# Kernel optimization log

Measured on AMD Instinct MI355X. Metric: run time of the kernel, lower is better.

The kernel has to match this reference:

```python
import jax, jax.numpy as jnp
import numpy as np
import math

# Config constants (from init_kwargs)
KV_CHANNELS = 128
NUM_HEADS = 32
NUM_KV_HEADS = 2
LAYER_NUMBER = 2  # apply_query_key_layer_scaling=True -> coeff = layer_number
HEAD_DIM = KV_CHANNELS
HIDDEN = KV_CHANNELS * NUM_HEADS
COEFF = float(LAYER_NUMBER)
NORM_FACTOR = math.sqrt(HEAD_DIM) * COEFF


def setup_inputs() -> dict:
    key = jax.random.key(0)
    k1, k2, k3, k4 = jax.random.split(key, 4)
    B, Q, KV = 2, 2048, 2048
    query_layer = jax.random.normal(k1, (B, NUM_HEADS, Q, HEAD_DIM), dtype=jnp.float32)
    key_layer = jax.random.normal(k2, (B, NUM_KV_HEADS, KV, HEAD_DIM), dtype=jnp.float32)
    value_layer = jax.random.normal(k3, (B, NUM_KV_HEADS, KV, HEAD_DIM), dtype=jnp.float32)
    attention_mask = jax.random.normal(k4, (B, 1, Q, KV), dtype=jnp.float32)
    return {
        "query_layer": query_layer,
        "key_layer": key_layer,
        "value_layer": value_layer,
        "attention_mask": attention_mask,
    }


def reference(query_layer, key_layer, value_layer, attention_mask):
    # Fallback (non-FusedSDPA) path of CoreAttention.forward, eval mode (no dropout).
    b, h, q_len, d = query_layer.shape
    g = key_layer.shape[1]          # num_key_value_heads
    r = h // g                      # n_rep
    # gaudi_chatglm_repeat_kv: grouped view (b, g, r, q, d) vs kv (b, g, kv, d)
    qg = query_layer.reshape(b, g, r, q_len, d)
    # scores: (b, g, r, q, kv)
    scores = jnp.einsum("bgrqd,bgkd->bgrqk", qg, key_layer) / NORM_FACTOR
    scores = scores * COEFF
    # mask unsqueezed at dim 1 -> (b, 1, 1, q, kv), broadcast-add
    scores = scores + attention_mask[:, None]
    # softmax in fp32, cast back to query dtype
    attn = jax.nn.softmax(scores.astype(jnp.float32), axis=-1).astype(query_layer.dtype)
    # AV: (b, g, r, q, d)
    out = jnp.einsum("bgrqk,bgkd->bgrqd", attn, value_layer)
    out = out.reshape(b, h, q_len, d)
    # permute (2,0,1,3) -> (q, b, h, d); reshape -> (q, b, hidden)
    context = jnp.transpose(out, (2, 0, 1, 3)).reshape(q_len, b, h * d)
    return context
```

## Files before the change

kernel.cpp:

```cpp
#include <hip/hip_runtime.h>
#include <hip/hip_bf16.h>


constexpr int Bn = 2, Hn = 32, Gn = 2, Qn = 2048, KVn = 2048, Dn = 128;
constexpr int WAVES = 8, QBLK = 32, HO = 8;
constexpr int KVB = 32, NT = KVn / KVB;
constexpr int NT32 = KVn / 32;
constexpr float SCALE = 0.08838834764831843f;
constexpr float L2E = 1.4426950408889634f;
constexpr float SCALE2 = SCALE * L2E;

constexpr size_t WSK_BYTES = (size_t)Bn * Gn * KVn * 256;

typedef __attribute__((ext_vector_type(16))) float f32x16;
typedef __attribute__((ext_vector_type(8))) __bf16 bf16x8;

__device__ __forceinline__ unsigned pk2(float a, float b) {
  union { __bf16 h[2]; unsigned u; } x;
  x.h[0] = (__bf16)a; x.h[1] = (__bf16)b;
  return x.u;
}

__global__ __launch_bounds__(256)
void prepack(const float* __restrict__ Kg, const float* __restrict__ Vg,
             char* __restrict__ wsK, char* __restrict__ wsV) {
  const int i = blockIdx.x * 256 + threadIdx.x;
  {
    const int dp = i & 63, kv = (i >> 6) & (KVn - 1), bg = i >> 17;
    const float* src = Kg + ((size_t)bg * KVn + kv) * Dn + 2 * dp;
    const unsigned pr = pk2(src[0], src[1]);
    const size_t off = (size_t)bg * (KVn * 256) + (size_t)kv * 256
                       + ((4 * dp) ^ ((kv & 15) << 4));
    *(unsigned*)(wsK + off) = pr;
  }
  {
    const int d = i & 127, vg = (i >> 7) & 1023, bg = i >> 17;
    const int t = vg >> 4, vkp = vg & 15;
    const float* src = Vg + ((size_t)bg * KVn + t * 32 + 2 * vkp) * Dn + d;
    const unsigned pr = pk2(src[0], src[Dn]);
    const int slot = (((d >> 3) ^ (d >> 1)) & 3) << 4;
    const size_t off = ((size_t)bg * NT32 + t) * 8192 + (d << 6)
                       + ((vkp * 4) ^ slot);
    *(unsigned*)(wsV + off) = pr;
  }
}

__global__ __launch_bounds__(512, 2)
void attn_fwd(const float* __restrict__ Qg, const float* __restrict__ Mg,
              const char* __restrict__ wsK, const char* __restrict__ wsV,
              float* __restrict__ Og) {
  __shared__ __align__(16) short Ks[2][KVB * Dn];
  __shared__ __align__(16) short Vt[2][Dn * KVB];
  __shared__ __align__(16) float Ms[2][QBLK * KVB];

  const int tid = threadIdx.x;
  const int lane = tid & 63, w = tid >> 6;
  const int hi = lane >> 5, ln = lane & 31;
  const int qb = blockIdx.x * QBLK, ho = blockIdx.y, b = blockIdx.z;
  const int h = ho * HO + w;
  const int g = ho >> 1, bg = b * Gn + g;

  bf16x8 aq[8];
  {
    const float* qr = Qg + ((size_t)(b * Hn + h) * Qn + qb + ln) * Dn + hi * 8;
#pragma unroll
    for (int ks = 0; ks < 8; ++ks) {
      float4 f0 = *(const float4*)(qr + ks * 16);
      float4 f1 = *(const float4*)(qr + ks * 16 + 4);
      union { unsigned u[4]; bf16x8 b; } t;
      t.u[0] = pk2(f0.x * SCALE2, f0.y * SCALE2);
      t.u[1] = pk2(f0.z * SCALE2, f0.w * SCALE2);
      t.u[2] = pk2(f1.x * SCALE2, f1.y * SCALE2);
      t.u[3] = pk2(f1.z * SCALE2, f1.w * SCALE2);
      aq[ks] = t.b;
    }
  }

  const char* wsKb = wsK + (size_t)bg * (KVn * 256);
  const char* wsVb = wsV + (size_t)bg * (KVn * 256);
  const int mr = (w & 3) * 8 + (lane >> 3);
  const int mc = (lane & 7) << 4;
  const char* mSrcBase = (const char*)Mg + (size_t)(b * Qn + qb + mr) * (KVn * 4)
                         + (mc ^ ((mr & 7) << 4));

  auto stage = [&](int tile, int buf) {
    if (w < 4) {
      const char* sk = wsKb + (size_t)tile * 8192 + w * 2048 + lane * 16;
      char* dk = (char*)Ks[buf] + w * 2048;
      __builtin_amdgcn_global_load_lds(
          (const __attribute__((address_space(1))) void*)sk,
          (__attribute__((address_space(3))) void*)dk, 16, 0, 0);
      __builtin_amdgcn_global_load_lds(
          (const __attribute__((address_space(1))) void*)(sk + 1024),
          (__attribute__((address_space(3))) void*)(dk + 1024), 16, 0, 0);
      const char* sm = mSrcBase + tile * 128;
      char* dm = (char*)Ms[buf] + w * 1024;
      __builtin_amdgcn_global_load_lds(
          (const __attribute__((address_space(1))) void*)sm,
          (__attribute__((address_space(3))) void*)dm, 16, 0, 0);
    } else {
      const int wv = w - 4;
      const char* sv = wsVb + (size_t)tile * 8192 + wv * 2048 + lane * 16;
      char* dv = (char*)Vt[buf] + wv * 2048;
      __builtin_amdgcn_global_load_lds(
          (const __attribute__((address_space(1))) void*)sv,
          (__attribute__((address_space(3))) void*)dv, 16, 0, 0);
      __builtin_amdgcn_global_load_lds(
          (const __attribute__((address_space(1))) void*)(sv + 1024),
          (__attribute__((address_space(3))) void*)(dv + 1024), 16, 0, 0);
    }
  };

  f32x16 o[4];
#pragma unroll
  for (int nt = 0; nt < 4; ++nt)
#pragma unroll
    for (int e = 0; e < 16; ++e) o[nt][e] = 0.0f;
  float lsum = 0.0f;

  stage(0, 0);
  __syncthreads();

  const int ksw = (ln & 15) << 4;
  const int msw = (ln & 7) << 4;

  for (int t = 0; t < NT; ++t) {
    const int cur = t & 1;
    const int tn = (t + 1 < NT) ? t + 1 : t;

    stage(tn, cur ^ 1);
    __builtin_amdgcn_sched_barrier(0);

    f32x16 s;
#pragma unroll
    for (int e = 0; e < 16; ++e) s[e] = 0.0f;
    const char* ksb = (const char*)Ks[cur];
    __builtin_amdgcn_s_setprio(1);
#pragma unroll
    for (int ks = 0; ks < 8; ++ks) {
      bf16x8 k0 = *(const bf16x8*)(ksb + (ln << 8) + ((ks * 32 + hi * 16) ^ ksw));
      s = __builtin_amdgcn_mfma_f32_32x32x16_bf16(k0, aq[ks], s, 0, 0, 0);
    }
    __builtin_amdgcn_s_setprio(0);

    const char* msb = (const char*)Ms[cur] + ln * 128;
    unsigned own[8];
    float psum = 0.0f;
#pragma unroll
    for (int gq = 0; gq < 4; ++gq) {
      float4 mkq = *(const float4*)(msb + ((gq * 32 + hi * 16) ^ msw));
      float p0 = __builtin_exp2f(__builtin_fmaf(mkq.x, L2E, s[4 * gq + 0]));
      float p1 = __builtin_exp2f(__builtin_fmaf(mkq.y, L2E, s[4 * gq + 1]));
      float p2 = __builtin_exp2f(__builtin_fmaf(mkq.z, L2E, s[4 * gq + 2]));
      float p3 = __builtin_exp2f(__builtin_fmaf(mkq.w, L2E, s[4 * gq + 3]));
      psum += (p0 + p1) + (p2 + p3);
      own[2 * gq] = pk2(p0, p1);
      own[2 * gq + 1] = pk2(p2, p3);
    }
    lsum += psum;

    unsigned sw[8];
#pragma unroll
    for (int i = 0; i < 8; ++i) sw[i] = __shfl_xor(own[i], 32);
    union Frag { unsigned u[4]; bf16x8 b; };
    Frag pf[2];
#pragma unroll
    for (int ks = 0; ks < 2; ++ks) {
      const int bsl = ks * 4;
      pf[ks].u[0] = hi ? sw[bsl + 2] : own[bsl + 0];
      pf[ks].u[1] = hi ? sw[bsl + 3] : own[bsl + 1];
      pf[ks].u[2] = hi ? own[bsl + 2] : sw[bsl + 0];
      pf[ks].u[3] = hi ? own[bsl + 3] : sw[bsl + 1];
    }

    const char* vtb = (const char*)Vt[cur];
    __builtin_amdgcn_s_setprio(1);
#pragma unroll
    for (int nt = 0; nt < 4; ++nt) {
      const int d = nt * 32 + ln;
      const int swz = (((d >> 3) ^ (d >> 1)) & 3) << 4;
#pragma unroll
      for (int ks = 0; ks < 2; ++ks) {
        bf16x8 vfr = *(const bf16x8*)(vtb + (d << 6) + (((ks * 32 + hi * 16)) ^ swz));
        o[nt] = __builtin_amdgcn_mfma_f32_32x32x16_bf16(vfr, pf[ks].b, o[nt], 0, 0, 0);
      }
    }
    __builtin_amdgcn_s_setprio(0);

    __syncthreads();
  }

  const float ltot = lsum + __shfl_xor(lsum, 32);
  const float invl = 1.0f / ltot;
  float* outp = Og + (size_t)(qb + ln) * (Bn * Hn * Dn) + (size_t)b * (Hn * Dn) + h * Dn;
#pragma unroll
  for (int nt = 0; nt < 4; ++nt)
#pragma unroll
    for (int gq = 0; gq < 4; ++gq) {
      float4 v;
      v.x = o[nt][gq * 4 + 0] * invl;
      v.y = o[nt][gq * 4 + 1] * invl;
      v.z = o[nt][gq * 4 + 2] * invl;
      v.w = o[nt][gq * 4 + 3] * invl;
      *(float4*)(outp + nt * 32 + gq * 8 + hi * 4) = v;
    }
}

extern "C" void kernel_launch(void* const* d_in, const int* in_sizes, int n_in,
                              void* d_out, int out_size, void* d_ws, size_t ws_size,
                              hipStream_t stream) {
  const float* q = (const float*)d_in[0];
  const float* k = (const float*)d_in[1];
  const float* v = (const float*)d_in[2];
  const float* m = (const float*)d_in[3];
  float* out = (float*)d_out;
  char* wsK = (char*)d_ws;
  char* wsV = wsK + WSK_BYTES;

  prepack<<<dim3((Bn * Gn * KVn * 64) / 256), 256, 0, stream>>>(k, v, wsK, wsV);
  dim3 grid(Qn / QBLK, Hn / HO, Bn);
  attn_fwd<<<grid, WAVES * 64, 0, stream>>>(q, m, wsK, wsV, out);
}
```

Measured before the change: 229.8 us.

## Double KV tile to 64 per iteration and use permlane32_swap for P fragments

Raises the KV tile processed per loop iteration from 32 to 64, halving the number of iterations and block-wide barriers. Every wave now stages K, V and mask slices instead of splitting roles. The two QK score accumulators are computed back to back, exposing more independent MFMA work. The lane-half exchange for P fragments uses the permlane32_swap builtin when available in place of shfl_xor plus selects. Shared memory doubles to about 64 KB per block, which may limit occupancy at the two-blocks-per-CU launch bound, and register pressure rises.

```diff
diff --git a/kernel.cpp b/kernel.cpp
--- a/kernel.cpp
+++ b/kernel.cpp
@@ -4,7 +4,7 @@
 
 constexpr int Bn = 2, Hn = 32, Gn = 2, Qn = 2048, KVn = 2048, Dn = 128;
 constexpr int WAVES = 8, QBLK = 32, HO = 8;
-constexpr int KVB = 32, NT = KVn / KVB;
+constexpr int KVB = 64, NT = KVn / KVB;
 constexpr int NT32 = KVn / 32;
 constexpr float SCALE = 0.08838834764831843f;
 constexpr float L2E = 1.4426950408889634f;
@@ -14,6 +14,7 @@
 
 typedef __attribute__((ext_vector_type(16))) float f32x16;
 typedef __attribute__((ext_vector_type(8))) __bf16 bf16x8;
+typedef __attribute__((ext_vector_type(2))) unsigned u32x2;
 
 __device__ __forceinline__ unsigned pk2(float a, float b) {
   union { __bf16 h[2]; unsigned u; } x;
@@ -78,37 +79,33 @@
 
   const char* wsKb = wsK + (size_t)bg * (KVn * 256);
   const char* wsVb = wsV + (size_t)bg * (KVn * 256);
-  const int mr = (w & 3) * 8 + (lane >> 3);
-  const int mc = (lane & 7) << 4;
+  const int mr = w * 4 + (lane >> 4);
+  const int mc = (lane & 15) << 4;
   const char* mSrcBase = (const char*)Mg + (size_t)(b * Qn + qb + mr) * (KVn * 4)
-                         + (mc ^ ((mr & 7) << 4));
+                         + (mc ^ ((mr & 15) << 4));
 
   auto stage = [&](int tile, int buf) {
-    if (w < 4) {
-      const char* sk = wsKb + (size_t)tile * 8192 + w * 2048 + lane * 16;
-      char* dk = (char*)Ks[buf] + w * 2048;
-      __builtin_amdgcn_global_load_lds(
-          (const __attribute__((address_space(1))) void*)sk,
-          (__attribute__((address_space(3))) void*)dk, 16, 0, 0);
-      __builtin_amdgcn_global_load_lds(
-          (const __attribute__((address_space(1))) void*)(sk + 1024),
-          (__attribute__((address_space(3))) void*)(dk + 1024), 16, 0, 0);
-      const char* sm = mSrcBase + tile * 128;
-      char* dm = (char*)Ms[buf] + w * 1024;
-      __builtin_amdgcn_global_load_lds(
-          (const __attribute__((address_space(1))) void*)sm,
-          (__attribute__((address_space(3))) void*)dm, 16, 0, 0);
-    } else {
-      const int wv = w - 4;
-      const char* sv = wsVb + (size_t)tile * 8192 + wv * 2048 + lane * 16;
-      char* dv = (char*)Vt[buf] + wv * 2048;
-      __builtin_amdgcn_global_load_lds(
-          (const __attribute__((address_space(1))) void*)sv,
-          (__attribute__((address_space(3))) void*)dv, 16, 0, 0);
-      __builtin_amdgcn_global_load_lds(
-          (const __attribute__((address_space(1))) void*)(sv + 1024),
-          (__attribute__((address_space(3))) void*)(dv + 1024), 16, 0, 0);
-    }
+    const char* sk = wsKb + (size_t)tile * 16384 + w * 2048 + lane * 16;
+    char* dk = (char*)Ks[buf] + w * 2048;
+    __builtin_amdgcn_global_load_lds(
+        (const __attribute__((address_space(1))) void*)sk,
+        (__attribute__((address_space(3))) void*)dk, 16, 0, 0);
+    __builtin_amdgcn_global_load_lds(
+        (const __attribute__((address_space(1))) void*)(sk + 1024),
+        (__attribute__((address_space(3))) void*)(dk + 1024), 16, 0, 0);
+    const char* sv = wsVb + (size_t)tile * 16384 + w * 2048 + lane * 16;
+    char* dv = (char*)Vt[buf] + w * 2048;
+    __builtin_amdgcn_global_load_lds(
+        (const __attribute__((address_space(1))) void*)sv,
+        (__attribute__((address_space(3))) void*)dv, 16, 0, 0);
+    __builtin_amdgcn_global_load_lds(
+        (const __attribute__((address_space(1))) void*)(sv + 1024),
+        (__attribute__((address_space(3))) void*)(dv + 1024), 16, 0, 0);
+    const char* sm = mSrcBase + tile * 256;
+    char* dm = (char*)Ms[buf] + w * 1024;
+    __builtin_amdgcn_global_load_lds(
+        (const __attribute__((address_space(1))) void*)sm,
+        (__attribute__((address_space(3))) void*)dm, 16, 0, 0);
   };
 
   f32x16 o[4];
@@ -122,7 +119,7 @@
   __syncthreads();
 
   const int ksw = (ln & 15) << 4;
-  const int msw = (ln & 7) << 4;
+  const int msw = (ln & 15) << 4;
 
   for (int t = 0; t < NT; ++t) {
     const int cur = t & 1;
@@ -131,46 +128,61 @@
     stage(tn, cur ^ 1);
     __builtin_amdgcn_sched_barrier(0);
 
-    f32x16 s;
-#pragma unroll
-    for (int e = 0; e < 16; ++e) s[e] = 0.0f;
+    f32x16 s0, s1;
+#pragma unroll
+    for (int e = 0; e < 16; ++e) { s0[e] = 0.0f; s1[e] = 0.0f; }
     const char* ksb = (const char*)Ks[cur];
     __builtin_amdgcn_s_setprio(1);
 #pragma unroll
     for (int ks = 0; ks < 8; ++ks) {
-      bf16x8 k0 = *(const bf16x8*)(ksb + (ln << 8) + ((ks * 32 + hi * 16) ^ ksw));
-      s = __builtin_amdgcn_mfma_f32_32x32x16_bf16(k0, aq[ks], s, 0, 0, 0);
+      const int byte = (ks * 32 + hi * 16) ^ ksw;
+      bf16x8 k0 = *(const bf16x8*)(ksb + (ln << 8) + byte);
+      bf16x8 k1 = *(const bf16x8*)(ksb + ((32 + ln) << 8) + byte);
+      s0 = __builtin_amdgcn_mfma_f32_32x32x16_bf16(k0, aq[ks], s0, 0, 0, 0);
+      s1 = __builtin_amdgcn_mfma_f32_32x32x16_bf16(k1, aq[ks], s1, 0, 0, 0);
     }
     __builtin_amdgcn_s_setprio(0);
 
-    const char* msb = (const char*)Ms[cur] + ln * 128;
-    unsigned own[8];
+    const char* msb = (const char*)Ms[cur] + ln * 256;
+    unsigned own0[8], own1[8];
     float psum = 0.0f;
 #pragma unroll
     for (int gq = 0; gq < 4; ++gq) {
-      float4 mkq = *(const float4*)(msb + ((gq * 32 + hi * 16) ^ msw));
-      float p0 = __builtin_exp2f(__builtin_fmaf(mkq.x, L2E, s[4 * gq + 0]));
-      float p1 = __builtin_exp2f(__builtin_fmaf(mkq.y, L2E, s[4 * gq + 1]));
-      float p2 = __builtin_exp2f(__builtin_fmaf(mkq.z, L2E, s[4 * gq + 2]));
-      float p3 = __builtin_exp2f(__builtin_fmaf(mkq.w, L2E, s[4 * gq + 3]));
-      psum += (p0 + p1) + (p2 + p3);
-      own[2 * gq] = pk2(p0, p1);
-      own[2 * gq + 1] = pk2(p2, p3);
+      float4 m0 = *(const float4*)(msb + ((gq * 32 + hi * 16) ^ msw));
+      float4 m1 = *(const float4*)(msb + ((128 + gq * 32 + hi * 16) ^ msw));
+      float p0 = __builtin_exp2f(__builtin_fmaf(m0.x, L2E, s0[4 * gq + 0]));
+      float p1 = __builtin_exp2f(__builtin_fmaf(m0.y, L2E, s0[4 * gq + 1]));
+      float p2 = __builtin_exp2f(__builtin_fmaf(m0.z, L2E, s0[4 * gq + 2]));
+      float p3 = __builtin_exp2f(__builtin_fmaf(m0.w, L2E, s0[4 * gq + 3]));
+      float q0 = __builtin_exp2f(__builtin_fmaf(m1.x, L2E, s1[4 * gq + 0]));
+      float q1 = __builtin_exp2f(__builtin_fmaf(m1.y, L2E, s1[4 * gq + 1]));
+      float q2 = __builtin_exp2f(__builtin_fmaf(m1.z, L2E, s1[4 * gq + 2]));
+      float q3 = __builtin_exp2f(__builtin_fmaf(m1.w, L2E, s1[4 * gq + 3]));
+      psum += ((p0 + p1) + (p2 + p3)) + ((q0 + q1) + (q2 + q3));
+      own0[2 * gq] = pk2(p0, p1); own0[2 * gq + 1] = pk2(p2, p3);
+      own1[2 * gq] = pk2(q0, q1); own1[2 * gq + 1] = pk2(q2, q3);
     }
     lsum += psum;
 
-    unsigned sw[8];
-#pragma unroll
-    for (int i = 0; i < 8; ++i) sw[i] = __shfl_xor(own[i], 32);
     union Frag { unsigned u[4]; bf16x8 b; };
-    Frag pf[2];
-#pragma unroll
-    for (int ks = 0; ks < 2; ++ks) {
-      const int bsl = ks * 4;
-      pf[ks].u[0] = hi ? sw[bsl + 2] : own[bsl + 0];
-      pf[ks].u[1] = hi ? sw[bsl + 3] : own[bsl + 1];
-      pf[ks].u[2] = hi ? own[bsl + 2] : sw[bsl + 0];
-      pf[ks].u[3] = hi ? own[bsl + 3] : sw[bsl + 1];
+    Frag pf[4];
+#pragma unroll
+    for (int ks = 0; ks < 4; ++ks) {
+      const unsigned* ow = (ks < 2) ? own0 : own1;
+      const int bsl = (ks & 1) * 4;
+#if __has_builtin(__builtin_amdgcn_permlane32_swap)
+      u32x2 r0 = __builtin_amdgcn_permlane32_swap(ow[bsl + 0], ow[bsl + 2], false, false);
+      u32x2 r1 = __builtin_amdgcn_permlane32_swap(ow[bsl + 1], ow[bsl + 3], false, false);
+      pf[ks].u[0] = r0.x; pf[ks].u[2] = r0.y;
+      pf[ks].u[1] = r1.x; pf[ks].u[3] = r1.y;
+#else
+      unsigned sA = __shfl_xor(ow[bsl + 0], 32), sC = __shfl_xor(ow[bsl + 2], 32);
+      unsigned sB = __shfl_xor(ow[bsl + 1], 32), sD = __shfl_xor(ow[bsl + 3], 32);
+      pf[ks].u[0] = hi ? sC : ow[bsl + 0];
+      pf[ks].u[1] = hi ? sD : ow[bsl + 1];
+      pf[ks].u[2] = hi ? ow[bsl + 2] : sA;
+      pf[ks].u[3] = hi ? ow[bsl + 3] : sB;
+#endif
     }
 
     const char* vtb = (const char*)Vt[cur];
@@ -180,8 +192,9 @@
       const int d = nt * 32 + ln;
       const int swz = (((d >> 3) ^ (d >> 1)) & 3) << 4;
 #pragma unroll
-      for (int ks = 0; ks < 2; ++ks) {
-        bf16x8 vfr = *(const bf16x8*)(vtb + (d << 6) + (((ks * 32 + hi * 16)) ^ swz));
+      for (int ks = 0; ks < 4; ++ks) {
+        const int base = (ks >> 1) * 8192 + (d << 6);
+        bf16x8 vfr = *(const bf16x8*)(vtb + base + (((ks & 1) * 32 + hi * 16) ^ swz));
         o[nt] = __builtin_amdgcn_mfma_f32_32x32x16_bf16(vfr, pf[ks].b, o[nt], 0, 0, 0);
       }
     }
```

After: 228.3 us. Within noise of the previous version (-0.7%).
